# Optimization experiments

Hardware: AMD Instinct MI355X
Metric: run time of the kernel (lower is better)

The kernel has to match this reference:

```python
import jax, jax.numpy as jnp
import numpy as np

LAMBDA_COORD = 5.0
LAMBDA_NOOBJ = 0.5
CELL_SILE = 1.0 / 7.0


def setup_inputs() -> dict:
    key = jax.random.key(0)
    k1, k2, k3 = jax.random.split(key, 3)
    B, S, C = 16384, 49, 30
    predictions = jax.random.normal(k1, (B, S, C), dtype=jnp.float32)
    targets = jax.random.uniform(k2, (B, S, C), dtype=jnp.float32)
    # confidence column must be exactly 0/1 for the equality masks in the loss
    obj = (jax.random.uniform(k3, (B, S)) < 0.3).astype(jnp.float32)
    targets = targets.at[:, :, 4].set(obj)
    return {"predictions": predictions, "targets": targets}


def reference(predictions, targets):
    # Flatten cells: row-major order matches torch boolean indexing order.
    p = predictions.reshape(-1, 30)  # [N, 30], N = B*49
    t = targets.reshape(-1, 30)
    conf = t[:, 4]
    coord_mask = conf == 1.0
    noobj = (conf == 0.0).astype(p.dtype)

    # no-object confidence loss on columns [4, 9]
    noobj_loss = LAMBDA_NOOBJ * jnp.sum(
        noobj * ((p[:, 4] - t[:, 4]) ** 2 + (p[:, 9] - t[:, 9]) ** 2))

    # The original zips N_obj rows against N_obj//2 output rows, so only the
    # first floor(N_obj/2) object cells (in flattened order) contribute.
    n_obj = jnp.sum(coord_mask.astype(jnp.int32))
    rank = jnp.cumsum(coord_mask.astype(jnp.int32))  # 1-indexed object rank
    w = (coord_mask & (rank <= n_obj // 2)).astype(p.dtype)

    # pred boxes: columns [0:4] and [5:9] -> [N, 2, 4]
    pb = p[:, :10].reshape(-1, 2, 5)[..., :4]
    # faithful in-place transform: a = xy*c - wh ; b = a*c + wh
    pa = pb[..., :2] * CELL_SILE - pb[..., 2:4]
    pbb = pa * CELL_SILE + pb[..., 2:4]
    pbox = jnp.concatenate([pa, pbb], axis=-1)  # [N, 2, 4]

    tb = jnp.square(t[:, :4])
    ta = tb[:, :2] * CELL_SILE - tb[:, 2:4]
    tbb = ta * CELL_SILE + tb[:, 2:4]
    tbox = jnp.concatenate([ta, tbb], axis=-1)  # [N, 4]

    # torchvision.ops.box_iou, batched over cells
    lt = jnp.maximum(pbox[..., :2], tbox[:, None, :2])
    rb = jnp.minimum(pbox[..., 2:], tbox[:, None, 2:])
    whd = jnp.clip(rb - lt, 0.0)
    inter = whd[..., 0] * whd[..., 1]  # [N, 2]
    area_p = (pbox[..., 2] - pbox[..., 0]) * (pbox[..., 3] - pbox[..., 1])
    area_t = (tbox[:, 2] - tbox[:, 0]) * (tbox[:, 3] - tbox[:, 1])
    iou = inter / (area_p + area_t[:, None] - inter)  # [N, 2]

    idx = jnp.argmax(iou, axis=1)  # responsible box per cell
    sel = jnp.take_along_axis(p[:, :10].reshape(-1, 2, 5),
                              idx[:, None, None], axis=1)[:, 0, :]  # [N, 5]
    obj_idx = jnp.argmax(t[:, 10:], axis=1)
    sel_cls = jnp.take_along_axis(p[:, 10:], obj_idx[:, None], axis=1)[:, 0]

    center = jnp.sum(w * jnp.sum((sel[:, :2] - t[:, :2]) ** 2, axis=1))
    xywh = jnp.sum(w * jnp.sum((sel[:, 2:4] - t[:, 2:4]) ** 2, axis=1))
    # original compares column 5 twice (confidence_loss and classier_loss are
    # the same term): pred class prob vs constant 1
    conf_l = jnp.sum(w * (sel_cls - 1.0) ** 2)
    cls_l = jnp.sum(w * (sel_cls - 1.0) ** 2)

    return LAMBDA_COORD * (center + xywh + conf_l + cls_l) + noobj_loss
```

## Files before the change

### kernel.cpp

```cpp
#include <hip/hip_runtime.h>


#define COLS 30
#define NB   3136

#define ROW_MATH_BODY                                                        \
    const float C = 1.0f / 7.0f;                                             \
    float conf = b2.x;                         \
    coord = (conf == 1.0f);                                                  \
    noo = 0.0f;                                                              \
    if (conf == 0.0f) {                                                      \
        float d4_ = a2.x - conf;                                             \
        float d9_ = a4.y - b4.y;                                             \
        noo = d4_ * d4_ + d9_ * d9_;                                         \
    }                                                                        \
    float T0 = b0.x, T1 = b0.y, T2v = b1.x, T3 = b1.y;                       \
    float tb0 = T0 * T0, tb1 = T1 * T1, tb2 = T2v * T2v, tb3 = T3 * T3;      \
    float tax = tb0 * C - tb2, tay = tb1 * C - tb3;                          \
    float tbx = tax * C + tb2, tby = tay * C + tb3;                          \
    float areaT = (tbx - tax) * (tby - tay);                                 \
    float pax0 = a0.x * C - a1.x, pay0 = a0.y * C - a1.y;                    \
    float pbx0 = pax0 * C + a1.x, pby0 = pay0 * C + a1.y;                    \
    float pax1 = a2.y * C - a3.y, pay1 = a3.x * C - a4.x;                    \
    float pbx1 = pax1 * C + a3.y, pby1 = pay1 * C + a4.x;                    \
    float ltx = fmaxf(pax0, tax), lty = fmaxf(pay0, tay);                    \
    float rbx = fminf(pbx0, tbx), rby = fminf(pby0, tby);                    \
    float wx = fmaxf(rbx - ltx, 0.0f), wy = fmaxf(rby - lty, 0.0f);          \
    float inter = wx * wy;                                                   \
    float areaP = (pbx0 - pax0) * (pby0 - pay0);                             \
    float iou0 = inter / (areaP + areaT - inter);                            \
    ltx = fmaxf(pax1, tax); lty = fmaxf(pay1, tay);                          \
    rbx = fminf(pbx1, tbx); rby = fminf(pby1, tby);                          \
    wx = fmaxf(rbx - ltx, 0.0f); wy = fmaxf(rby - lty, 0.0f);                \
    inter = wx * wy;                                                         \
    areaP = (pbx1 - pax1) * (pby1 - pay1);                                   \
    float iou1 = inter / (areaP + areaT - inter);                            \
    int idx = (iou1 > iou0) ? 1 : 0;              \
    float sx = idx ? a2.y : a0.x;                                            \
    float sy = idx ? a3.x : a0.y;                                            \
    float sw = idx ? a3.y : a1.x;                                            \
    float sh = idx ? a4.x : a1.y;                                            \
    float best = b5.x, pc = a5.x;                \
    CLS_STEP(b5.y,  a5.y)  CLS_STEP(b6.x,  a6.x)  CLS_STEP(b6.y,  a6.y)      \
    CLS_STEP(b7.x,  a7.x)  CLS_STEP(b7.y,  a7.y)  CLS_STEP(b8.x,  a8.x)      \
    CLS_STEP(b8.y,  a8.y)  CLS_STEP(b9.x,  a9.x)  CLS_STEP(b9.y,  a9.y)      \
    CLS_STEP(b10.x, a10.x) CLS_STEP(b10.y, a10.y) CLS_STEP(b11.x, a11.x)     \
    CLS_STEP(b11.y, a11.y) CLS_STEP(b12.x, a12.x) CLS_STEP(b12.y, a12.y)     \
    CLS_STEP(b13.x, a13.x) CLS_STEP(b13.y, a13.y) CLS_STEP(b14.x, a14.x)     \
    CLS_STEP(b14.y, a14.y)                                                   \
    float d0 = sx - T0, d1 = sy - T1, d2 = sw - T2v, d3 = sh - T3;           \
    float dc = pc - 1.0f;                                                    \
    r = d0 * d0 + d1 * d1 + d2 * d2 + d3 * d3 + 2.0f * dc * dc;

#define CLS_STEP(tv, pv) { float v_ = (tv); if (v_ > best) { best = v_; pc = (pv); } }

__device__ __forceinline__ void row_compute_vals(
    float2 a0, float2 a1, float2 a2, float2 a3, float2 a4,
    float2 a5, float2 a6, float2 a7, float2 a8, float2 a9,
    float2 a10, float2 a11, float2 a12, float2 a13, float2 a14,
    float2 b0, float2 b1, float2 b2, float2 b3, float2 b4,
    float2 b5, float2 b6, float2 b7, float2 b8, float2 b9,
    float2 b10, float2 b11, float2 b12, float2 b13, float2 b14,
    bool& coord, float& r, float& noo)
{
    ROW_MATH_BODY
}

__device__ __forceinline__ void row_load_compute(
    const float* __restrict__ gp, const float* __restrict__ gt, long row,
    bool& coord, float& r, float& noo)
{
    const float2* P2 = (const float2*)(gp + row * (long)COLS);
    const float2* T2 = (const float2*)(gt + row * (long)COLS);
    float2 a0 = P2[0],  a1 = P2[1],  a2 = P2[2],  a3 = P2[3],  a4 = P2[4];
    float2 a5 = P2[5],  a6 = P2[6],  a7 = P2[7],  a8 = P2[8],  a9 = P2[9];
    float2 a10 = P2[10], a11 = P2[11], a12 = P2[12], a13 = P2[13], a14 = P2[14];
    float2 b0 = T2[0],  b1 = T2[1],  b2 = T2[2],  b3 = T2[3],  b4 = T2[4];
    float2 b5 = T2[5],  b6 = T2[6],  b7 = T2[7],  b8 = T2[8],  b9 = T2[9];
    float2 b10 = T2[10], b11 = T2[11], b12 = T2[12], b13 = T2[13], b14 = T2[14];
    ROW_MATH_BODY
}

__global__ __launch_bounds__(256, 3) void yolo_k1(const float* __restrict__ gp,
                                                  const float* __restrict__ gt,
                                                  int* __restrict__ cnt,
                                                  float* __restrict__ sumR,
                                                  float* __restrict__ noo) {
    __shared__ float wr[4], wn[4];
    __shared__ int wc[4];
    int tid = threadIdx.x;
    long row = (long)blockIdx.x * 256 + tid;
    unsigned int voff = (unsigned int)(row * (long)(COLS * 4));

    float2 p0, p1, p2, p3, p4, p5, p6, p7, p8, p9, p10, p11, p12, p13, p14;
    float2 q0, q1, q2, q3, q4, q5, q6, q7, q8, q9, q10, q11, q12, q13, q14;
    asm volatile(
        "global_load_dwordx2 %0,  %[off], %[pb]\n\t"
        "global_load_dwordx2 %1,  %[off], %[pb] offset:8\n\t"
        "global_load_dwordx2 %2,  %[off], %[pb] offset:16\n\t"
        "global_load_dwordx2 %3,  %[off], %[pb] offset:24\n\t"
        "global_load_dwordx2 %4,  %[off], %[pb] offset:32\n\t"
        "global_load_dwordx2 %5,  %[off], %[pb] offset:40\n\t"
        "global_load_dwordx2 %6,  %[off], %[pb] offset:48\n\t"
        "global_load_dwordx2 %7,  %[off], %[pb] offset:56\n\t"
        "global_load_dwordx2 %8,  %[off], %[pb] offset:64\n\t"
        "global_load_dwordx2 %9,  %[off], %[pb] offset:72\n\t"
        "global_load_dwordx2 %10, %[off], %[pb] offset:80\n\t"
        "global_load_dwordx2 %11, %[off], %[pb] offset:88\n\t"
        "global_load_dwordx2 %12, %[off], %[pb] offset:96\n\t"
        "global_load_dwordx2 %13, %[off], %[pb] offset:104\n\t"
        "global_load_dwordx2 %14, %[off], %[pb] offset:112\n\t"
        "global_load_dwordx2 %15, %[off], %[tb]\n\t"
        "global_load_dwordx2 %16, %[off], %[tb] offset:8\n\t"
        "global_load_dwordx2 %17, %[off], %[tb] offset:16\n\t"
        "global_load_dwordx2 %18, %[off], %[tb] offset:24\n\t"
        "global_load_dwordx2 %19, %[off], %[tb] offset:32\n\t"
        "global_load_dwordx2 %20, %[off], %[tb] offset:40\n\t"
        "global_load_dwordx2 %21, %[off], %[tb] offset:48\n\t"
        "global_load_dwordx2 %22, %[off], %[tb] offset:56\n\t"
        "global_load_dwordx2 %23, %[off], %[tb] offset:64\n\t"
        "global_load_dwordx2 %24, %[off], %[tb] offset:72\n\t"
        "global_load_dwordx2 %25, %[off], %[tb] offset:80\n\t"
        "global_load_dwordx2 %26, %[off], %[tb] offset:88\n\t"
        "global_load_dwordx2 %27, %[off], %[tb] offset:96\n\t"
        "global_load_dwordx2 %28, %[off], %[tb] offset:104\n\t"
        "global_load_dwordx2 %29, %[off], %[tb] offset:112\n\t"
        "s_waitcnt vmcnt(0)"
        : "=v"(p0), "=v"(p1), "=v"(p2), "=v"(p3), "=v"(p4),
          "=v"(p5), "=v"(p6), "=v"(p7), "=v"(p8), "=v"(p9),
          "=v"(p10), "=v"(p11), "=v"(p12), "=v"(p13), "=v"(p14),
          "=v"(q0), "=v"(q1), "=v"(q2), "=v"(q3), "=v"(q4),
          "=v"(q5), "=v"(q6), "=v"(q7), "=v"(q8), "=v"(q9),
          "=v"(q10), "=v"(q11), "=v"(q12), "=v"(q13), "=v"(q14)
        : [off]"v"(voff), [pb]"s"(gp), [tb]"s"(gt)
        : "memory");

    bool coord; float r, nt;
    row_compute_vals(p0, p1, p2, p3, p4, p5, p6, p7, p8, p9,
                     p10, p11, p12, p13, p14,
                     q0, q1, q2, q3, q4, q5, q6, q7, q8, q9,
                     q10, q11, q12, q13, q14, coord, r, nt);
    float rl = coord ? r : 0.0f;

    unsigned long long bal = __ballot(coord);
    int c = (int)__popcll(bal);
#pragma unroll
    for (int off = 32; off > 0; off >>= 1) {
        rl += __shfl_down(rl, off);
        nt += __shfl_down(nt, off);
    }
    int wave = tid >> 6, lane = tid & 63;
    if (lane == 0) { wr[wave] = rl; wn[wave] = nt; wc[wave] = c; }
    __syncthreads();
    if (tid == 0) {
        cnt[blockIdx.x]  = wc[0] + wc[1] + wc[2] + wc[3];
        sumR[blockIdx.x] = wr[0] + wr[1] + wr[2] + wr[3];
        noo[blockIdx.x]  = wn[0] + wn[1] + wn[2] + wn[3];
    }
}

__global__ __launch_bounds__(256) void yolo_k2(const int* __restrict__ cnt,
                                               const float* __restrict__ sumR,
                                               const float* __restrict__ noo,
                                               const float* __restrict__ gp,
                                               const float* __restrict__ gt,
                                               float* __restrict__ out) {
    __shared__ int   wsum[4];
    __shared__ float wf[4], wn2[4];
    __shared__ int   s_bstar, s_kstar;
    __shared__ float s_base;
    __shared__ int   s_wcnt[4];
    int tid = threadIdx.x;
    int lane = tid & 63, wave = tid >> 6;
    if (tid == 0) { s_bstar = -1; s_kstar = 0; }

    const int PER = 13;
    int start = tid * PER;
    int end = min(NB, start + PER);

    int cloc = 0; float nloc = 0.0f;
    for (int i = start; i < end; ++i) { cloc += cnt[i]; nloc += noo[i]; }

    int incl = cloc;
#pragma unroll
    for (int off = 1; off < 64; off <<= 1) {
        int v = __shfl_up(incl, off);
        if (lane >= off) incl += v;
    }
    if (lane == 63) wsum[wave] = incl;
    __syncthreads();
    int woff = 0;
#pragma unroll
    for (int w = 0; w < 4; ++w) woff += (w < wave) ? wsum[w] : 0;
    int ex = woff + incl - cloc;
    int n_obj = wsum[0] + wsum[1] + wsum[2] + wsum[3];
    int n_half = n_obj >> 1;

    float acc = 0.0f;
    int running = ex;
    for (int i = start; i < end; ++i) {
        int ci = cnt[i];
        if (ci > 0) {
            if (running + ci <= n_half) {
                acc += sumR[i];
            } else if (running < n_half) {
                s_bstar = i;
                s_kstar = n_half - running;
            }
        }
        running += ci;
    }

#pragma unroll
    for (int off = 32; off > 0; off >>= 1) {
        acc  += __shfl_down(acc, off);
        nloc += __shfl_down(nloc, off);
    }
    if (lane == 0) { wf[wave] = acc; wn2[wave] = nloc; }
    __syncthreads();
    if (tid == 0)
        s_base = 5.0f * (wf[0] + wf[1] + wf[2] + wf[3])
               + 0.5f * (wn2[0] + wn2[1] + wn2[2] + wn2[3]);
    __syncthreads();

    int bstar = s_bstar, kstar = s_kstar;
    float total = 0.0f;
    if (bstar >= 0) {
        long row = (long)bstar * 256 + tid;
        bool coord; float r, nt;
        row_load_compute(gp, gt, row, coord, r, nt);
        unsigned long long bal = __ballot(coord);
        if (lane == 0) s_wcnt[wave] = (int)__popcll(bal);
        __syncthreads();
        int waveoff = 0;
#pragma unroll
        for (int w = 0; w < 4; ++w) waveoff += (w < wave) ? s_wcnt[w] : 0;
        unsigned long long below_incl =
            (lane == 63) ? bal : (bal & ((1ull << (lane + 1)) - 1ull));
        int rank = waveoff + (int)__popcll(below_incl);
        float val = (coord && rank <= kstar) ? r : 0.0f;
#pragma unroll
        for (int off = 32; off > 0; off >>= 1) val += __shfl_down(val, off);
        if (lane == 0) wf[wave] = val;
        __syncthreads();
        if (tid == 0) total = wf[0] + wf[1] + wf[2] + wf[3];
    }
    if (tid == 0) out[0] = s_base + 5.0f * total;
}

extern "C" void kernel_launch(void* const* d_in, const int* in_sizes, int n_in,
                              void* d_out, int out_size, void* d_ws, size_t ws_size,
                              hipStream_t stream) {
    (void)in_sizes; (void)n_in; (void)out_size; (void)ws_size;
    const float* p = (const float*)d_in[0];
    const float* t = (const float*)d_in[1];
    char* ws = (char*)d_ws;
    int*   cnt  = (int*)ws;
    float* sumR = (float*)(ws + (size_t)NB * 4);
    float* noo  = (float*)(ws + (size_t)NB * 8);
    float* out  = (float*)d_out;

    yolo_k1<<<NB, 256, 0, stream>>>(p, t, cnt, sumR, noo);
    yolo_k2<<<1, 256, 0, stream>>>(cnt, sumR, noo, p, t, out);
}
```

Measured before the change: 212.6 us.

## Stage row tiles through LDS with coalesced dwordx4 global loads

Each block now reads its contiguous 256-row slab of predictions and targets with fully coalesced 16-byte loads, writes it to shared memory, then each thread reads its own 30-float row back from LDS. Before, every thread issued 8-byte loads strided by 120 bytes, which coalesces poorly. The cost is about 60 KB of LDS per block plus a barrier, and the occupancy hint drops from 3 to 2 blocks per SIMD. Row reads from LDS at a 30-float stride may also cause bank conflicts.

```diff
diff --git a/kernel.cpp b/kernel.cpp
--- a/kernel.cpp
+++ b/kernel.cpp
@@ -3,6 +3,9 @@
 
 #define COLS 30
 #define NB   3136
+
+typedef float f32x4 __attribute__((ext_vector_type(4)));
+typedef float f32x2 __attribute__((ext_vector_type(2)));
 
 #define ROW_MATH_BODY                                                        \
     const float C = 1.0f / 7.0f;                                             \
@@ -81,65 +84,83 @@
     ROW_MATH_BODY
 }
 
-__global__ __launch_bounds__(256, 3) void yolo_k1(const float* __restrict__ gp,
+__global__ __launch_bounds__(256, 2) void yolo_k1(const float* __restrict__ gp,
                                                   const float* __restrict__ gt,
                                                   int* __restrict__ cnt,
                                                   float* __restrict__ sumR,
                                                   float* __restrict__ noo) {
+    __shared__ f32x4 ldsP[1920];
+    __shared__ f32x4 ldsT[1920];
     __shared__ float wr[4], wn[4];
     __shared__ int wc[4];
     int tid = threadIdx.x;
-    long row = (long)blockIdx.x * 256 + tid;
-    unsigned int voff = (unsigned int)(row * (long)(COLS * 4));
-
-    float2 p0, p1, p2, p3, p4, p5, p6, p7, p8, p9, p10, p11, p12, p13, p14;
-    float2 q0, q1, q2, q3, q4, q5, q6, q7, q8, q9, q10, q11, q12, q13, q14;
+
+    long gbase = (long)blockIdx.x * (256L * COLS);
+    const float* gpb = gp + gbase;
+    const float* gtb = gt + gbase;
+
+    unsigned o0 = (unsigned)tid * 16u + 4096u;
+    unsigned o1 = (unsigned)tid * 16u + 12288u;
+    unsigned o2 = (unsigned)tid * 16u + 20480u;
+    unsigned o3 = (unsigned)tid * 16u + 24576u;
+    unsigned o4 = (unsigned)tid * 8u  + 28672u;
+
+    f32x4 p0, p1, p2, p3, p4, p5, p6; f32x2 p7;
+    f32x4 t0, t1, t2, t3, t4, t5, t6; f32x2 t7;
     asm volatile(
-        "global_load_dwordx2 %0,  %[off], %[pb]\n\t"
-        "global_load_dwordx2 %1,  %[off], %[pb] offset:8\n\t"
-        "global_load_dwordx2 %2,  %[off], %[pb] offset:16\n\t"
-        "global_load_dwordx2 %3,  %[off], %[pb] offset:24\n\t"
-        "global_load_dwordx2 %4,  %[off], %[pb] offset:32\n\t"
-        "global_load_dwordx2 %5,  %[off], %[pb] offset:40\n\t"
-        "global_load_dwordx2 %6,  %[off], %[pb] offset:48\n\t"
-        "global_load_dwordx2 %7,  %[off], %[pb] offset:56\n\t"
-        "global_load_dwordx2 %8,  %[off], %[pb] offset:64\n\t"
-        "global_load_dwordx2 %9,  %[off], %[pb] offset:72\n\t"
-        "global_load_dwordx2 %10, %[off], %[pb] offset:80\n\t"
-        "global_load_dwordx2 %11, %[off], %[pb] offset:88\n\t"
-        "global_load_dwordx2 %12, %[off], %[pb] offset:96\n\t"
-        "global_load_dwordx2 %13, %[off], %[pb] offset:104\n\t"
-        "global_load_dwordx2 %14, %[off], %[pb] offset:112\n\t"
-        "global_load_dwordx2 %15, %[off], %[tb]\n\t"
-        "global_load_dwordx2 %16, %[off], %[tb] offset:8\n\t"
-        "global_load_dwordx2 %17, %[off], %[tb] offset:16\n\t"
-        "global_load_dwordx2 %18, %[off], %[tb] offset:24\n\t"
-        "global_load_dwordx2 %19, %[off], %[tb] offset:32\n\t"
-        "global_load_dwordx2 %20, %[off], %[tb] offset:40\n\t"
-        "global_load_dwordx2 %21, %[off], %[tb] offset:48\n\t"
-        "global_load_dwordx2 %22, %[off], %[tb] offset:56\n\t"
-        "global_load_dwordx2 %23, %[off], %[tb] offset:64\n\t"
-        "global_load_dwordx2 %24, %[off], %[tb] offset:72\n\t"
-        "global_load_dwordx2 %25, %[off], %[tb] offset:80\n\t"
-        "global_load_dwordx2 %26, %[off], %[tb] offset:88\n\t"
-        "global_load_dwordx2 %27, %[off], %[tb] offset:96\n\t"
-        "global_load_dwordx2 %28, %[off], %[tb] offset:104\n\t"
-        "global_load_dwordx2 %29, %[off], %[tb] offset:112\n\t"
+        "global_load_dwordx4 %0,  %[o0], %[pb] offset:-4096\n\t"
+        "global_load_dwordx4 %1,  %[o0], %[pb]\n\t"
+        "global_load_dwordx4 %2,  %[o1], %[pb] offset:-4096\n\t"
+        "global_load_dwordx4 %3,  %[o1], %[pb]\n\t"
+        "global_load_dwordx4 %4,  %[o2], %[pb] offset:-4096\n\t"
+        "global_load_dwordx4 %5,  %[o2], %[pb]\n\t"
+        "global_load_dwordx4 %6,  %[o3], %[pb]\n\t"
+        "global_load_dwordx2 %7,  %[o4], %[pb]\n\t"
+        "global_load_dwordx4 %8,  %[o0], %[tb] offset:-4096\n\t"
+        "global_load_dwordx4 %9,  %[o0], %[tb]\n\t"
+        "global_load_dwordx4 %10, %[o1], %[tb] offset:-4096\n\t"
+        "global_load_dwordx4 %11, %[o1], %[tb]\n\t"
+        "global_load_dwordx4 %12, %[o2], %[tb] offset:-4096\n\t"
+        "global_load_dwordx4 %13, %[o2], %[tb]\n\t"
+        "global_load_dwordx4 %14, %[o3], %[tb]\n\t"
+        "global_load_dwordx2 %15, %[o4], %[tb]\n\t"
         "s_waitcnt vmcnt(0)"
-        : "=v"(p0), "=v"(p1), "=v"(p2), "=v"(p3), "=v"(p4),
-          "=v"(p5), "=v"(p6), "=v"(p7), "=v"(p8), "=v"(p9),
-          "=v"(p10), "=v"(p11), "=v"(p12), "=v"(p13), "=v"(p14),
-          "=v"(q0), "=v"(q1), "=v"(q2), "=v"(q3), "=v"(q4),
-          "=v"(q5), "=v"(q6), "=v"(q7), "=v"(q8), "=v"(q9),
-          "=v"(q10), "=v"(q11), "=v"(q12), "=v"(q13), "=v"(q14)
-        : [off]"v"(voff), [pb]"s"(gp), [tb]"s"(gt)
+        : "=&v"(p0), "=&v"(p1), "=&v"(p2), "=&v"(p3), "=&v"(p4), "=&v"(p5),
+          "=&v"(p6), "=&v"(p7),
+          "=&v"(t0), "=&v"(t1), "=&v"(t2), "=&v"(t3), "=&v"(t4), "=&v"(t5),
+          "=&v"(t6), "=&v"(t7)
+        : [o0]"v"(o0), [o1]"v"(o1), [o2]"v"(o2), [o3]"v"(o3), [o4]"v"(o4),
+          [pb]"s"(gpb), [tb]"s"(gtb)
         : "memory");
 
+    ldsP[0 * 256 + tid] = p0;  ldsP[1 * 256 + tid] = p1;
+    ldsP[2 * 256 + tid] = p2;  ldsP[3 * 256 + tid] = p3;
+    ldsP[4 * 256 + tid] = p4;  ldsP[5 * 256 + tid] = p5;
+    ldsP[6 * 256 + tid] = p6;
+    ldsT[0 * 256 + tid] = t0;  ldsT[1 * 256 + tid] = t1;
+    ldsT[2 * 256 + tid] = t2;  ldsT[3 * 256 + tid] = t3;
+    ldsT[4 * 256 + tid] = t4;  ldsT[5 * 256 + tid] = t5;
+    ldsT[6 * 256 + tid] = t6;
+    float* lpf = (float*)ldsP;
+    float* ltf = (float*)ldsT;
+    *(f32x2*)(lpf + 7168 + 2 * tid) = p7;
+    *(f32x2*)(ltf + 7168 + 2 * tid) = t7;
+    __syncthreads();
+
+    const float2* P2 = (const float2*)(lpf + tid * COLS);
+    const float2* T2 = (const float2*)(ltf + tid * COLS);
+    float2 a0 = P2[0],  a1 = P2[1],  a2 = P2[2],  a3 = P2[3],  a4 = P2[4];
+    float2 a5 = P2[5],  a6 = P2[6],  a7 = P2[7],  a8 = P2[8],  a9 = P2[9];
+    float2 a10 = P2[10], a11 = P2[11], a12 = P2[12], a13 = P2[13], a14 = P2[14];
+    float2 b0 = T2[0],  b1 = T2[1],  b2 = T2[2],  b3 = T2[3],  b4 = T2[4];
+    float2 b5 = T2[5],  b6 = T2[6],  b7 = T2[7],  b8 = T2[8],  b9 = T2[9];
+    float2 b10 = T2[10], b11 = T2[11], b12 = T2[12], b13 = T2[13], b14 = T2[14];
+
     bool coord; float r, nt;
-    row_compute_vals(p0, p1, p2, p3, p4, p5, p6, p7, p8, p9,
-                     p10, p11, p12, p13, p14,
-                     q0, q1, q2, q3, q4, q5, q6, q7, q8, q9,
-                     q10, q11, q12, q13, q14, coord, r, nt);
+    row_compute_vals(a0, a1, a2, a3, a4, a5, a6, a7, a8, a9,
+                     a10, a11, a12, a13, a14,
+                     b0, b1, b2, b3, b4, b5, b6, b7, b8, b9,
+                     b10, b11, b12, b13, b14, coord, r, nt);
     float rl = coord ? r : 0.0f;
 
     unsigned long long bal = __ballot(coord);
```

Result: no change. 209.5 us (-1.5%).

## Stage rows through LDS with coalesced loads, one wave per tile

Applied to the files above, without the earlier changes.

Instead of each thread loading its own 120-byte row with strided dwordx2 loads, each wave now loads a 64-row chunk with fully coalesced float2 loads into LDS, then reads its row back from LDS to compute. Each wave handles 256 rows in four sequential 64-row steps, and blocks shrink to two waves, which removes the cross-wave shared-memory reduction and __syncthreads. The aim is better global memory coalescing. In exchange it adds LDS traffic, possible bank conflicts from the stride-15 row reads, and serialized per-step loads.

```diff
diff --git a/kernel.cpp b/kernel.cpp
--- a/kernel.cpp
+++ b/kernel.cpp
@@ -3,6 +3,9 @@
 
 #define COLS 30
 #define NB   3136
+
+typedef float f32x4 __attribute__((ext_vector_type(4)));
+typedef float f32x2 __attribute__((ext_vector_type(2)));
 
 #define ROW_MATH_BODY                                                        \
     const float C = 1.0f / 7.0f;                                             \
@@ -81,81 +84,68 @@
     ROW_MATH_BODY
 }
 
-__global__ __launch_bounds__(256, 3) void yolo_k1(const float* __restrict__ gp,
+__global__ __launch_bounds__(128, 3) void yolo_k1(const float* __restrict__ gp,
                                                   const float* __restrict__ gt,
                                                   int* __restrict__ cnt,
                                                   float* __restrict__ sumR,
-                                                  float* __restrict__ noo) {
-    __shared__ float wr[4], wn[4];
-    __shared__ int wc[4];
-    int tid = threadIdx.x;
-    long row = (long)blockIdx.x * 256 + tid;
-    unsigned int voff = (unsigned int)(row * (long)(COLS * 4));
-
-    float2 p0, p1, p2, p3, p4, p5, p6, p7, p8, p9, p10, p11, p12, p13, p14;
-    float2 q0, q1, q2, q3, q4, q5, q6, q7, q8, q9, q10, q11, q12, q13, q14;
-    asm volatile(
-        "global_load_dwordx2 %0,  %[off], %[pb]\n\t"
-        "global_load_dwordx2 %1,  %[off], %[pb] offset:8\n\t"
-        "global_load_dwordx2 %2,  %[off], %[pb] offset:16\n\t"
-        "global_load_dwordx2 %3,  %[off], %[pb] offset:24\n\t"
-        "global_load_dwordx2 %4,  %[off], %[pb] offset:32\n\t"
-        "global_load_dwordx2 %5,  %[off], %[pb] offset:40\n\t"
-        "global_load_dwordx2 %6,  %[off], %[pb] offset:48\n\t"
-        "global_load_dwordx2 %7,  %[off], %[pb] offset:56\n\t"
-        "global_load_dwordx2 %8,  %[off], %[pb] offset:64\n\t"
-        "global_load_dwordx2 %9,  %[off], %[pb] offset:72\n\t"
-        "global_load_dwordx2 %10, %[off], %[pb] offset:80\n\t"
-        "global_load_dwordx2 %11, %[off], %[pb] offset:88\n\t"
-        "global_load_dwordx2 %12, %[off], %[pb] offset:96\n\t"
-        "global_load_dwordx2 %13, %[off], %[pb] offset:104\n\t"
-        "global_load_dwordx2 %14, %[off], %[pb] offset:112\n\t"
-        "global_load_dwordx2 %15, %[off], %[tb]\n\t"
-        "global_load_dwordx2 %16, %[off], %[tb] offset:8\n\t"
-        "global_load_dwordx2 %17, %[off], %[tb] offset:16\n\t"
-        "global_load_dwordx2 %18, %[off], %[tb] offset:24\n\t"
-        "global_load_dwordx2 %19, %[off], %[tb] offset:32\n\t"
-        "global_load_dwordx2 %20, %[off], %[tb] offset:40\n\t"
-        "global_load_dwordx2 %21, %[off], %[tb] offset:48\n\t"
-        "global_load_dwordx2 %22, %[off], %[tb] offset:56\n\t"
-        "global_load_dwordx2 %23, %[off], %[tb] offset:64\n\t"
-        "global_load_dwordx2 %24, %[off], %[tb] offset:72\n\t"
-        "global_load_dwordx2 %25, %[off], %[tb] offset:80\n\t"
-        "global_load_dwordx2 %26, %[off], %[tb] offset:88\n\t"
-        "global_load_dwordx2 %27, %[off], %[tb] offset:96\n\t"
-        "global_load_dwordx2 %28, %[off], %[tb] offset:104\n\t"
-        "global_load_dwordx2 %29, %[off], %[tb] offset:112\n\t"
-        "s_waitcnt vmcnt(0)"
-        : "=v"(p0), "=v"(p1), "=v"(p2), "=v"(p3), "=v"(p4),
-          "=v"(p5), "=v"(p6), "=v"(p7), "=v"(p8), "=v"(p9),
-          "=v"(p10), "=v"(p11), "=v"(p12), "=v"(p13), "=v"(p14),
-          "=v"(q0), "=v"(q1), "=v"(q2), "=v"(q3), "=v"(q4),
-          "=v"(q5), "=v"(q6), "=v"(q7), "=v"(q8), "=v"(q9),
-          "=v"(q10), "=v"(q11), "=v"(q12), "=v"(q13), "=v"(q14)
-        : [off]"v"(voff), [pb]"s"(gp), [tb]"s"(gt)
-        : "memory");
-
-    bool coord; float r, nt;
-    row_compute_vals(p0, p1, p2, p3, p4, p5, p6, p7, p8, p9,
-                     p10, p11, p12, p13, p14,
-                     q0, q1, q2, q3, q4, q5, q6, q7, q8, q9,
-                     q10, q11, q12, q13, q14, coord, r, nt);
-    float rl = coord ? r : 0.0f;
-
-    unsigned long long bal = __ballot(coord);
-    int c = (int)__popcll(bal);
-#pragma unroll
-    for (int off = 32; off > 0; off >>= 1) {
-        rl += __shfl_down(rl, off);
-        nt += __shfl_down(nt, off);
-    }
-    int wave = tid >> 6, lane = tid & 63;
-    if (lane == 0) { wr[wave] = rl; wn[wave] = nt; wc[wave] = c; }
-    __syncthreads();
-    if (tid == 0) {
-        cnt[blockIdx.x]  = wc[0] + wc[1] + wc[2] + wc[3];
-        sumR[blockIdx.x] = wr[0] + wr[1] + wr[2] + wr[3];
-        noo[blockIdx.x]  = wn[0] + wn[1] + wn[2] + wn[3];
+                                                  float* __restrict__ noo_out) {
+    __shared__ float2 lds2[2][1920];
+    int tid  = threadIdx.x;
+    int lane = tid & 63;
+    int wib  = tid >> 6;
+    int t    = blockIdx.x * 2 + wib;
+    if (t >= NB) return;
+
+    float2* L = lds2[wib];
+    const float2* P2g = (const float2*)gp;
+    const float2* T2g = (const float2*)gt;
+
+    float sumA = 0.0f, nooA = 0.0f;
+    int   cntA = 0;
+
+    for (int s = 0; s < 4; ++s) {
+        int base = 3840 * t + 960 * s + lane;
+        float2 vp[15], vt[15];
+#pragma unroll
+        for (int m = 0; m < 15; ++m) vp[m] = P2g[base + 64 * m];
+#pragma unroll
+        for (int m = 0; m < 15; ++m) vt[m] = T2g[base + 64 * m];
+#pragma unroll
+        for (int m = 0; m < 15; ++m) L[m * 64 + lane] = vp[m];
+#pragma unroll
+        for (int m = 0; m < 15; ++m) L[960 + m * 64 + lane] = vt[m];
+
+        const float2* Pr = &L[lane * 15];
+        const float2* Tr = &L[960 + lane * 15];
+        float2 a0 = Pr[0],  a1 = Pr[1],  a2 = Pr[2],  a3 = Pr[3],  a4 = Pr[4];
+        float2 a5 = Pr[5],  a6 = Pr[6],  a7 = Pr[7],  a8 = Pr[8],  a9 = Pr[9];
+        float2 a10 = Pr[10], a11 = Pr[11], a12 = Pr[12], a13 = Pr[13], a14 = Pr[14];
+        float2 b0 = Tr[0],  b1 = Tr[1],  b2 = Tr[2],  b3 = Tr[3],  b4 = Tr[4];
+        float2 b5 = Tr[5],  b6 = Tr[6],  b7 = Tr[7],  b8 = Tr[8],  b9 = Tr[9];
+        float2 b10 = Tr[10], b11 = Tr[11], b12 = Tr[12], b13 = Tr[13], b14 = Tr[14];
+
+        bool coord; float r, nt;
+        row_compute_vals(a0, a1, a2, a3, a4, a5, a6, a7, a8, a9,
+                         a10, a11, a12, a13, a14,
+                         b0, b1, b2, b3, b4, b5, b6, b7, b8, b9,
+                         b10, b11, b12, b13, b14, coord, r, nt);
+        float rl = coord ? r : 0.0f;
+
+        unsigned long long bal = __ballot(coord);
+        int c = (int)__popcll(bal);
+#pragma unroll
+        for (int off = 32; off > 0; off >>= 1) {
+            rl += __shfl_down(rl, off);
+            nt += __shfl_down(nt, off);
+        }
+        cntA += c;
+        sumA += rl;
+        nooA += nt;
+    }
+    if (lane == 0) {
+        cnt[t]     = cntA;
+        sumR[t]    = sumA;
+        noo_out[t] = nooA;
     }
 }
 
@@ -260,6 +250,6 @@
     float* noo  = (float*)(ws + (size_t)NB * 8);
     float* out  = (float*)d_out;
 
-    yolo_k1<<<NB, 256, 0, stream>>>(p, t, cnt, sumR, noo);
+    yolo_k1<<<NB / 2, 128, 0, stream>>>(p, t, cnt, sumR, noo);
     yolo_k2<<<1, 256, 0, stream>>>(cnt, sumR, noo, p, t, out);
 }
```

After: 219.1 us. 3.0% more time.
